# Performance work log

Hardware: AMD Instinct MI355X
Metric: run time of the kernel (lower is better)

Reference implementation:

```python
import jax, jax.numpy as jnp
import numpy as np

DIM_MODEL = 1024
DIM_K = 1024
DIM_V = 1024


def setup_inputs() -> dict:
    key = jax.random.key(0)
    ks = jax.random.split(key, 7)
    B, S = 4, 2048
    scale = 1.0 / np.sqrt(DIM_MODEL)
    return {
        "x": jax.random.normal(ks[0], (B, S, DIM_MODEL), dtype=jnp.float32),
        # weights stored [in, out] (transpose of torch Linear.weight)
        "Wq": jax.random.normal(ks[1], (DIM_MODEL, DIM_K), dtype=jnp.float32) * scale,
        "Wk": jax.random.normal(ks[2], (DIM_MODEL, DIM_K), dtype=jnp.float32) * scale,
        "Wv": jax.random.normal(ks[3], (DIM_MODEL, DIM_V), dtype=jnp.float32) * scale,
        "Wo": jax.random.normal(ks[4], (DIM_V, DIM_MODEL), dtype=jnp.float32) * (1.0 / np.sqrt(DIM_V)),
        "ln2_gamma": jnp.ones((DIM_MODEL,), dtype=jnp.float32),
        "ln2_beta": jnp.zeros((DIM_MODEL,), dtype=jnp.float32),
    }


def _layernorm(x, gamma, beta, eps=1e-5):
    mu = jnp.mean(x, axis=-1, keepdims=True)
    var = jnp.var(x, axis=-1, keepdims=True)
    return (x - mu) * jax.lax.rsqrt(var + eps) * gamma + beta


def reference(x, Wq, Wk, Wv, Wo, ln2_gamma, ln2_beta):
    # single-head attention, x: [B,S,D]
    q = jnp.einsum("bsd,dk->bsk", x, Wq)
    k = jnp.einsum("bsd,dk->bsk", x, Wk)
    v = jnp.einsum("bsd,dv->bsv", x, Wv)
    scores = jnp.einsum("bqk,bsk->bqs", q, k) / jnp.sqrt(jnp.asarray(DIM_K, x.dtype))
    attn = jax.nn.softmax(scores, axis=-1)  # [B,S,S]
    ctx = jnp.einsum("bqs,bsv->bqv", attn, v)
    hidden = jnp.einsum("bqv,vd->bqd", ctx, Wo)
    hidden = _layernorm(hidden, ln2_gamma, ln2_beta)
    return hidden
```

## Files before the change

### kernel.cpp

```cpp
#include <hip/hip_runtime.h>
#include <hip/hip_bf16.h>
#include <stdint.h>

typedef __bf16 bf16;
typedef __attribute__((ext_vector_type(8))) __bf16 bf16x8;
typedef __attribute__((ext_vector_type(4))) __bf16 bf16x4;
typedef __attribute__((ext_vector_type(4))) float f32x4;

#define AS1 __attribute__((address_space(1)))
#define AS3 __attribute__((address_space(3)))

__device__ __forceinline__ void gl_lds16(const void* g, void* l) {
  __builtin_amdgcn_global_load_lds((const AS1 uint32_t*)g, (AS3 uint32_t*)l, 16, 0, 0);
}

template <typename OUT, int MODE>
__global__ __launch_bounds__(256) void gemm_bt(
    const bf16* __restrict__ Abase, const bf16* __restrict__ Bbase,
    OUT* __restrict__ Cbase, int K, int lda, int ldb, int ldc,
    long long sA, long long sB, long long sC, float alpha,
    float* __restrict__ lsum) {
  __shared__ bf16 As[128 * 64];
  __shared__ bf16 Bs[128 * 64];
  const int z = blockIdx.z;
  const bf16* A = Abase + (long long)z * sA;
  const bf16* B = Bbase + (long long)z * sB;
  OUT* C = Cbase + (long long)z * sC;
  const int m0 = blockIdx.y * 128, n0 = blockIdx.x * 128;
  const int t = threadIdx.x;
  const int lane = t & 63, wave = t >> 6;
  const int wm = (wave >> 1) * 64, wn = (wave & 1) * 64;
  const int quad = lane >> 4, r = lane & 15;

  const int srow = t >> 3;
  const int schunk = (t & 7) ^ (srow & 7);
  const bf16* ga = A + (long long)(m0 + srow) * lda + schunk * 8;
  const bf16* gb = B + (long long)(n0 + srow) * ldb + schunk * 8;
  char* la = (char*)As + t * 16;
  char* lb = (char*)Bs + t * 16;

  f32x4 acc[4][4] = {};

  for (int k0 = 0; k0 < K; k0 += 64) {
    __syncthreads();
#pragma unroll
    for (int rd = 0; rd < 4; rd++) {
      gl_lds16(ga + (long long)(32 * rd) * lda, la + rd * 4096);
      gl_lds16(gb + (long long)(32 * rd) * ldb, lb + rd * 4096);
    }
    ga += 64;
    gb += 64;
    __syncthreads();

#pragma unroll
    for (int kk = 0; kk < 2; kk++) {
      bf16x8 af[4], bfr[4];
      const int csa = ((kk * 4 + quad) ^ (r & 7)) * 16;
      const char* pa = (const char*)As + (wm + r) * 128 + csa;
      const char* pb = (const char*)Bs + (wn + r) * 128 + csa;
#pragma unroll
      for (int i = 0; i < 4; i++) af[i] = *(const bf16x8*)(pa + i * 2048);
#pragma unroll
      for (int j = 0; j < 4; j++) bfr[j] = *(const bf16x8*)(pb + j * 2048);
#pragma unroll
      for (int i = 0; i < 4; i++)
#pragma unroll
        for (int j = 0; j < 4; j++)
          acc[i][j] = __builtin_amdgcn_mfma_f32_16x16x32_bf16(af[i], bfr[j],
                                                              acc[i][j], 0, 0, 0);
    }
  }

#pragma unroll
  for (int i = 0; i < 4; i++) {
    const int row0 = m0 + wm + i * 16 + quad * 4;
    float rsum[4] = {0.f, 0.f, 0.f, 0.f};
    float inv[4];
    if constexpr (MODE == 2) {
#pragma unroll
      for (int rg = 0; rg < 4; rg++)
        inv[rg] = 1.f / lsum[(long long)z * 2048 + row0 + rg];
    }
#pragma unroll
    for (int j = 0; j < 4; j++) {
      const int col = n0 + wn + j * 16 + r;
#pragma unroll
      for (int rg = 0; rg < 4; rg++) {
        float v = acc[i][j][rg] * alpha;
        if constexpr (MODE == 1) {
          bf16 eb = (bf16)__expf(v);
          C[(long long)(row0 + rg) * ldc + col] = (OUT)eb;
          rsum[rg] += (float)eb;
        } else if constexpr (MODE == 2) {
          C[(long long)(row0 + rg) * ldc + col] = (OUT)(v * inv[rg]);
        } else {
          C[(long long)(row0 + rg) * ldc + col] = (OUT)v;
        }
      }
    }
    if constexpr (MODE == 1) {
#pragma unroll
      for (int rg = 0; rg < 4; rg++) {
#pragma unroll
        for (int off = 8; off >= 1; off >>= 1)
          rsum[rg] += __shfl_xor(rsum[rg], off);
        if (r == 0)
          atomicAdd(&lsum[(long long)z * 2048 + row0 + rg], rsum[rg]);
      }
    }
  }
}

__global__ __launch_bounds__(256) void cvt_f32_bf16(
    const float* __restrict__ in, bf16* __restrict__ out, long long n8,
    float* __restrict__ lsum) {
  if (blockIdx.x < 32) lsum[blockIdx.x * 256 + threadIdx.x] = 0.f;
  long long i = (long long)blockIdx.x * 256 + threadIdx.x;
  if (i >= n8) return;
  const float4* p = (const float4*)in;
  float4 a = p[i * 2], b = p[i * 2 + 1];
  bf16x8 o;
  o[0] = (bf16)a.x; o[1] = (bf16)a.y; o[2] = (bf16)a.z; o[3] = (bf16)a.w;
  o[4] = (bf16)b.x; o[5] = (bf16)b.y; o[6] = (bf16)b.z; o[7] = (bf16)b.w;
  ((bf16x8*)out)[i] = o;
}

__global__ __launch_bounds__(256) void transpose_w4(
    const float* __restrict__ Wq, const float* __restrict__ Wk,
    const float* __restrict__ Wv, const float* __restrict__ Wo,
    bf16* __restrict__ Wcat, bf16* __restrict__ Wot) {
  __shared__ float tile[32][33];
  const int z = blockIdx.z;
  const float* W = (z == 0) ? Wq : (z == 1) ? Wk : (z == 2) ? Wv : Wo;
  bf16* dst = (z < 3) ? (Wcat + (long long)z * 1024 * 1024) : Wot;
  int bx = blockIdx.x * 32, by = blockIdx.y * 32;
  int tx = threadIdx.x & 31, ty = threadIdx.x >> 5;
#pragma unroll
  for (int i = 0; i < 32; i += 8)
    tile[ty + i][tx] = W[(long long)(by + ty + i) * 1024 + bx + tx];
  __syncthreads();
#pragma unroll
  for (int i = 0; i < 32; i += 8)
    dst[(long long)(bx + ty + i) * 1024 + by + tx] = (bf16)tile[tx][ty + i];
}

__global__ __launch_bounds__(256) void transpose_v(
    const bf16* __restrict__ V, bf16* __restrict__ Vt, int ldsrc,
    long long sV) {
  __shared__ bf16 tile[32][33];
  const bf16* Vb = V + (long long)blockIdx.z * sV;
  bf16* Vtb = Vt + (long long)blockIdx.z * 1024 * 2048;
  int bx = blockIdx.x * 32, by = blockIdx.y * 32;
  int tx = threadIdx.x & 31, ty = threadIdx.x >> 5;
#pragma unroll
  for (int i = 0; i < 32; i += 8)
    tile[ty + i][tx] = Vb[(long long)(by + ty + i) * ldsrc + bx + tx];
  __syncthreads();
#pragma unroll
  for (int i = 0; i < 32; i += 8)
    Vtb[(long long)(bx + ty + i) * 2048 + by + tx] = tile[tx][ty + i];
}

__global__ __launch_bounds__(256) void layernorm_rows(
    const bf16* __restrict__ H, const float* __restrict__ gamma,
    const float* __restrict__ beta, float* __restrict__ O) {
  const long long row = blockIdx.x;
  const bf16* h = H + row * 1024;
  float* o = O + row * 1024;
  const int t = threadIdx.x;
  const int lane = t & 63, wave = t >> 6;
  bf16x4 hv = ((const bf16x4*)h)[t];
  float v[4] = {(float)hv[0], (float)hv[1], (float)hv[2], (float)hv[3]};
  float s = v[0] + v[1] + v[2] + v[3];
  float ss = v[0] * v[0] + v[1] * v[1] + v[2] * v[2] + v[3] * v[3];
#pragma unroll
  for (int off = 32; off >= 1; off >>= 1) {
    s += __shfl_xor(s, off);
    ss += __shfl_xor(ss, off);
  }
  __shared__ float rs[4], rss[4];
  if (lane == 0) {
    rs[wave] = s;
    rss[wave] = ss;
  }
  __syncthreads();
  s = rs[0] + rs[1] + rs[2] + rs[3];
  ss = rss[0] + rss[1] + rss[2] + rss[3];
  const float mean = s * (1.f / 1024.f);
  const float var = ss * (1.f / 1024.f) - mean * mean;
  const float rstd = rsqrtf(var + 1e-5f);
  float4 g = ((const float4*)gamma)[t];
  float4 bb = ((const float4*)beta)[t];
  float4 rr;
  rr.x = (v[0] - mean) * rstd * g.x + bb.x;
  rr.y = (v[1] - mean) * rstd * g.y + bb.y;
  rr.z = (v[2] - mean) * rstd * g.z + bb.z;
  rr.w = (v[3] - mean) * rstd * g.w + bb.w;
  ((float4*)o)[t] = rr;
}

extern "C" void kernel_launch(void* const* d_in, const int* in_sizes, int n_in,
                              void* d_out, int out_size, void* d_ws,
                              size_t ws_size, hipStream_t stream) {
  const float* x = (const float*)d_in[0];
  const float* Wq = (const float*)d_in[1];
  const float* Wk = (const float*)d_in[2];
  const float* Wv = (const float*)d_in[3];
  const float* Wo = (const float*)d_in[4];
  const float* gamma = (const float*)d_in[5];
  const float* beta = (const float*)d_in[6];
  float* out = (float*)d_out;

  char* ws = (char*)d_ws;
  const size_t MB = 1024ull * 1024ull;
  bf16* Xb = (bf16*)(ws + 0);
  bf16* Wcat = (bf16*)(ws + 16 * MB);
  bf16* Wot = (bf16*)(ws + 22 * MB);
  bf16* QKV = (bf16*)(ws + 24 * MB);
  bf16* Vt = (bf16*)(ws + 72 * MB);
  bf16* expS = (bf16*)(ws + 88 * MB);
  float* lsum = (float*)(ws + 120 * MB);
  bf16* ctx = (bf16*)(ws + 121 * MB);
  bf16* Hd = (bf16*)(ws + 137 * MB);

  const long long bQKV = 2048LL * 3072;

  cvt_f32_bf16<<<4096, 256, 0, stream>>>(x, Xb, 8192LL * 1024 / 8, lsum);
  transpose_w4<<<dim3(32, 32, 4), 256, 0, stream>>>(Wq, Wk, Wv, Wo, Wcat, Wot);

  gemm_bt<bf16, 0><<<dim3(24, 64, 1), 256, 0, stream>>>(
      Xb, Wcat, QKV, 1024, 1024, 1024, 3072, 0, 0, 0, 1.f, nullptr);

  transpose_v<<<dim3(32, 64, 4), 256, 0, stream>>>(QKV + 2048, Vt, 3072, bQKV);

  gemm_bt<bf16, 1><<<dim3(16, 16, 4), 256, 0, stream>>>(
      QKV, QKV + 1024, expS, 1024, 3072, 3072, 2048, bQKV, bQKV,
      2048 * 2048LL, 0.03125f, lsum);

  gemm_bt<bf16, 2><<<dim3(8, 16, 4), 256, 0, stream>>>(
      expS, Vt, ctx, 2048, 2048, 2048, 1024, 2048 * 2048LL, 1024 * 2048LL,
      2048 * 1024LL, 1.f, lsum);

  gemm_bt<bf16, 0><<<dim3(8, 64, 1), 256, 0, stream>>>(
      ctx, Wot, Hd, 1024, 1024, 1024, 1024, 0, 0, 0, 1.f, nullptr);

  layernorm_rows<<<8192, 256, 0, stream>>>(Hd, gamma, beta, out);
}
```

Baseline: 311.9 us.

## Fuse V transpose into QKV GEMM, merge prep kernels, use 64-row tiles

The QKV GEMM epilogue now writes V-column blocks transposed into Vt through an LDS staging tile, which removes the separate transpose_v kernel and its extra read and write of V. The input conversion and the weight transposes are merged into one prep launch to save a kernel launch. The PV and output-projection GEMMs switch to a 64x128 tile kernel, doubling the grid size to improve CU occupancy on the small-grid GEMMs. In exchange the QKV GEMM does extra LDS work and an extra sync for the V blocks, and the smaller tiles reuse less data per block.

Measured after the change: 301.9 us. 3.2% less time.

```diff
diff --git a/kernel.cpp b/kernel.cpp
--- a/kernel.cpp
+++ b/kernel.cpp
@@ -14,18 +14,17 @@
   __builtin_amdgcn_global_load_lds((const AS1 uint32_t*)g, (AS3 uint32_t*)l, 16, 0, 0);
 }
 
-template <typename OUT, int MODE>
-__global__ __launch_bounds__(256) void gemm_bt(
+template <int MODE>
+__global__ __launch_bounds__(256) void gemm128(
     const bf16* __restrict__ Abase, const bf16* __restrict__ Bbase,
-    OUT* __restrict__ Cbase, int K, int lda, int ldb, int ldc,
+    bf16* __restrict__ Cbase, int K, int lda, int ldb, int ldc,
     long long sA, long long sB, long long sC, float alpha,
-    float* __restrict__ lsum) {
-  __shared__ bf16 As[128 * 64];
-  __shared__ bf16 Bs[128 * 64];
+    float* __restrict__ lsum, bf16* __restrict__ Vt) {
+  extern __shared__ char smem[];
   const int z = blockIdx.z;
   const bf16* A = Abase + (long long)z * sA;
   const bf16* B = Bbase + (long long)z * sB;
-  OUT* C = Cbase + (long long)z * sC;
+  bf16* C = Cbase + (long long)z * sC;
   const int m0 = blockIdx.y * 128, n0 = blockIdx.x * 128;
   const int t = threadIdx.x;
   const int lane = t & 63, wave = t >> 6;
@@ -36,8 +35,8 @@
   const int schunk = (t & 7) ^ (srow & 7);
   const bf16* ga = A + (long long)(m0 + srow) * lda + schunk * 8;
   const bf16* gb = B + (long long)(n0 + srow) * ldb + schunk * 8;
-  char* la = (char*)As + t * 16;
-  char* lb = (char*)Bs + t * 16;
+  char* la = smem + t * 16;
+  char* lb = smem + 16384 + t * 16;
 
   f32x4 acc[4][4] = {};
 
@@ -56,8 +55,8 @@
     for (int kk = 0; kk < 2; kk++) {
       bf16x8 af[4], bfr[4];
       const int csa = ((kk * 4 + quad) ^ (r & 7)) * 16;
-      const char* pa = (const char*)As + (wm + r) * 128 + csa;
-      const char* pb = (const char*)Bs + (wn + r) * 128 + csa;
+      const char* pa = smem + (wm + r) * 128 + csa;
+      const char* pb = smem + 16384 + (wn + r) * 128 + csa;
 #pragma unroll
       for (int i = 0; i < 4; i++) af[i] = *(const bf16x8*)(pa + i * 2048);
 #pragma unroll
@@ -68,6 +67,36 @@
         for (int j = 0; j < 4; j++)
           acc[i][j] = __builtin_amdgcn_mfma_f32_16x16x32_bf16(af[i], bfr[j],
                                                               acc[i][j], 0, 0, 0);
+    }
+  }
+
+  if constexpr (MODE == 3) {
+    if (blockIdx.x >= 16) {
+      bf16* T = (bf16*)smem;
+      __syncthreads();
+#pragma unroll
+      for (int i = 0; i < 4; i++)
+#pragma unroll
+        for (int j = 0; j < 4; j++)
+#pragma unroll
+          for (int rg = 0; rg < 4; rg++) {
+            const int m = wm + i * 16 + quad * 4 + rg;
+            const int n = wn + j * 16 + r;
+            T[n * 136 + m] = (bf16)acc[i][j][rg];
+          }
+      __syncthreads();
+      const int v0 = n0 - 2048;
+      const int zz = m0 >> 11;
+      const int s0l = m0 & 2047;
+      bf16* Vtb = Vt + (long long)zz * 1024 * 2048;
+      const int c = t & 15;
+#pragma unroll
+      for (int p = 0; p < 8; p++) {
+        const int n = p * 16 + (t >> 4);
+        bf16x8 val = *(const bf16x8*)(T + n * 136 + c * 8);
+        *(bf16x8*)(Vtb + (long long)(v0 + n) * 2048 + s0l + c * 8) = val;
+      }
+      return;
     }
   }
 
@@ -89,12 +118,12 @@
         float v = acc[i][j][rg] * alpha;
         if constexpr (MODE == 1) {
           bf16 eb = (bf16)__expf(v);
-          C[(long long)(row0 + rg) * ldc + col] = (OUT)eb;
+          C[(long long)(row0 + rg) * ldc + col] = eb;
           rsum[rg] += (float)eb;
         } else if constexpr (MODE == 2) {
-          C[(long long)(row0 + rg) * ldc + col] = (OUT)(v * inv[rg]);
+          C[(long long)(row0 + rg) * ldc + col] = (bf16)(v * inv[rg]);
         } else {
-          C[(long long)(row0 + rg) * ldc + col] = (OUT)v;
+          C[(long long)(row0 + rg) * ldc + col] = (bf16)v;
         }
       }
     }
@@ -111,54 +140,120 @@
   }
 }
 
-__global__ __launch_bounds__(256) void cvt_f32_bf16(
-    const float* __restrict__ in, bf16* __restrict__ out, long long n8,
+template <int MODE>
+__global__ __launch_bounds__(256) void gemm64(
+    const bf16* __restrict__ Abase, const bf16* __restrict__ Bbase,
+    bf16* __restrict__ Cbase, int K, int lda, int ldb, int ldc,
+    long long sA, long long sB, long long sC, float alpha,
     float* __restrict__ lsum) {
-  if (blockIdx.x < 32) lsum[blockIdx.x * 256 + threadIdx.x] = 0.f;
-  long long i = (long long)blockIdx.x * 256 + threadIdx.x;
-  if (i >= n8) return;
-  const float4* p = (const float4*)in;
-  float4 a = p[i * 2], b = p[i * 2 + 1];
-  bf16x8 o;
-  o[0] = (bf16)a.x; o[1] = (bf16)a.y; o[2] = (bf16)a.z; o[3] = (bf16)a.w;
-  o[4] = (bf16)b.x; o[5] = (bf16)b.y; o[6] = (bf16)b.z; o[7] = (bf16)b.w;
-  ((bf16x8*)out)[i] = o;
-}
-
-__global__ __launch_bounds__(256) void transpose_w4(
-    const float* __restrict__ Wq, const float* __restrict__ Wk,
-    const float* __restrict__ Wv, const float* __restrict__ Wo,
-    bf16* __restrict__ Wcat, bf16* __restrict__ Wot) {
+  extern __shared__ char smem[];
+  const int z = blockIdx.z;
+  const bf16* A = Abase + (long long)z * sA;
+  const bf16* B = Bbase + (long long)z * sB;
+  bf16* C = Cbase + (long long)z * sC;
+  const int m0 = blockIdx.y * 64, n0 = blockIdx.x * 128;
+  const int t = threadIdx.x;
+  const int lane = t & 63, wave = t >> 6;
+  const int wm = (wave >> 1) * 32, wn = (wave & 1) * 64;
+  const int quad = lane >> 4, r = lane & 15;
+
+  const int srow = t >> 3;
+  const int schunk = (t & 7) ^ (srow & 7);
+  const bf16* ga = A + (long long)(m0 + srow) * lda + schunk * 8;
+  const bf16* gb = B + (long long)(n0 + srow) * ldb + schunk * 8;
+  char* la = smem + t * 16;
+  char* lb = smem + 8192 + t * 16;
+
+  f32x4 acc[2][4] = {};
+
+  for (int k0 = 0; k0 < K; k0 += 64) {
+    __syncthreads();
+#pragma unroll
+    for (int rd = 0; rd < 2; rd++)
+      gl_lds16(ga + (long long)(32 * rd) * lda, la + rd * 4096);
+#pragma unroll
+    for (int rd = 0; rd < 4; rd++)
+      gl_lds16(gb + (long long)(32 * rd) * ldb, lb + rd * 4096);
+    ga += 64;
+    gb += 64;
+    __syncthreads();
+
+#pragma unroll
+    for (int kk = 0; kk < 2; kk++) {
+      bf16x8 af[2], bfr[4];
+      const int csa = ((kk * 4 + quad) ^ (r & 7)) * 16;
+      const char* pa = smem + (wm + r) * 128 + csa;
+      const char* pb = smem + 8192 + (wn + r) * 128 + csa;
+#pragma unroll
+      for (int i = 0; i < 2; i++) af[i] = *(const bf16x8*)(pa + i * 2048);
+#pragma unroll
+      for (int j = 0; j < 4; j++) bfr[j] = *(const bf16x8*)(pb + j * 2048);
+#pragma unroll
+      for (int i = 0; i < 2; i++)
+#pragma unroll
+        for (int j = 0; j < 4; j++)
+          acc[i][j] = __builtin_amdgcn_mfma_f32_16x16x32_bf16(af[i], bfr[j],
+                                                              acc[i][j], 0, 0, 0);
+    }
+  }
+
+#pragma unroll
+  for (int i = 0; i < 2; i++) {
+    const int row0 = m0 + wm + i * 16 + quad * 4;
+    float inv[4];
+    if constexpr (MODE == 2) {
+#pragma unroll
+      for (int rg = 0; rg < 4; rg++)
+        inv[rg] = 1.f / lsum[(long long)z * 2048 + row0 + rg];
+    }
+#pragma unroll
+    for (int j = 0; j < 4; j++) {
+      const int col = n0 + wn + j * 16 + r;
+#pragma unroll
+      for (int rg = 0; rg < 4; rg++) {
+        float v = acc[i][j][rg] * alpha;
+        if constexpr (MODE == 2) v *= inv[rg];
+        C[(long long)(row0 + rg) * ldc + col] = (bf16)v;
+      }
+    }
+  }
+}
+
+__global__ __launch_bounds__(256) void prep(
+    const float* __restrict__ x, const float* __restrict__ Wq,
+    const float* __restrict__ Wk, const float* __restrict__ Wv,
+    const float* __restrict__ Wo, bf16* __restrict__ Xb,
+    bf16* __restrict__ Wcat, bf16* __restrict__ Wot,
+    float* __restrict__ lsum) {
   __shared__ float tile[32][33];
-  const int z = blockIdx.z;
-  const float* W = (z == 0) ? Wq : (z == 1) ? Wk : (z == 2) ? Wv : Wo;
-  bf16* dst = (z < 3) ? (Wcat + (long long)z * 1024 * 1024) : Wot;
-  int bx = blockIdx.x * 32, by = blockIdx.y * 32;
-  int tx = threadIdx.x & 31, ty = threadIdx.x >> 5;
-#pragma unroll
-  for (int i = 0; i < 32; i += 8)
-    tile[ty + i][tx] = W[(long long)(by + ty + i) * 1024 + bx + tx];
-  __syncthreads();
-#pragma unroll
-  for (int i = 0; i < 32; i += 8)
-    dst[(long long)(bx + ty + i) * 1024 + by + tx] = (bf16)tile[tx][ty + i];
-}
-
-__global__ __launch_bounds__(256) void transpose_v(
-    const bf16* __restrict__ V, bf16* __restrict__ Vt, int ldsrc,
-    long long sV) {
-  __shared__ bf16 tile[32][33];
-  const bf16* Vb = V + (long long)blockIdx.z * sV;
-  bf16* Vtb = Vt + (long long)blockIdx.z * 1024 * 2048;
-  int bx = blockIdx.x * 32, by = blockIdx.y * 32;
-  int tx = threadIdx.x & 31, ty = threadIdx.x >> 5;
-#pragma unroll
-  for (int i = 0; i < 32; i += 8)
-    tile[ty + i][tx] = Vb[(long long)(by + ty + i) * ldsrc + bx + tx];
-  __syncthreads();
-#pragma unroll
-  for (int i = 0; i < 32; i += 8)
-    Vtb[(long long)(bx + ty + i) * 2048 + by + tx] = tile[tx][ty + i];
+  const int bx = blockIdx.x;
+  const int t = threadIdx.x;
+  if (bx < 4096) {
+    if (bx < 32) lsum[bx * 256 + t] = 0.f;
+    long long i = (long long)bx * 256 + t;
+    const float4* p = (const float4*)x;
+    float4 a = p[i * 2], b = p[i * 2 + 1];
+    bf16x8 o;
+    o[0] = (bf16)a.x; o[1] = (bf16)a.y; o[2] = (bf16)a.z; o[3] = (bf16)a.w;
+    o[4] = (bf16)b.x; o[5] = (bf16)b.y; o[6] = (bf16)b.z; o[7] = (bf16)b.w;
+    ((bf16x8*)Xb)[i] = o;
+  } else {
+    int idx = bx - 4096;
+    const int zw = idx >> 10;
+    idx &= 1023;
+    const int tiy = idx >> 5, tix = idx & 31;
+    const float* W = (zw == 0) ? Wq : (zw == 1) ? Wk : (zw == 2) ? Wv : Wo;
+    bf16* dst = (zw < 3) ? (Wcat + (long long)zw * 1024 * 1024) : Wot;
+    const int bx0 = tix * 32, by0 = tiy * 32;
+    const int ttx = t & 31, tty = t >> 5;
+#pragma unroll
+    for (int i = 0; i < 32; i += 8)
+      tile[tty + i][ttx] = W[(long long)(by0 + tty + i) * 1024 + bx0 + ttx];
+    __syncthreads();
+#pragma unroll
+    for (int i = 0; i < 32; i += 8)
+      dst[(long long)(bx0 + tty + i) * 1024 + by0 + ttx] = (bf16)tile[ttx][tty + i];
+  }
 }
 
 __global__ __launch_bounds__(256) void layernorm_rows(
@@ -225,23 +320,20 @@
 
   const long long bQKV = 2048LL * 3072;
 
-  cvt_f32_bf16<<<4096, 256, 0, stream>>>(x, Xb, 8192LL * 1024 / 8, lsum);
-  transpose_w4<<<dim3(32, 32, 4), 256, 0, stream>>>(Wq, Wk, Wv, Wo, Wcat, Wot);
-
-  gemm_bt<bf16, 0><<<dim3(24, 64, 1), 256, 0, stream>>>(
-      Xb, Wcat, QKV, 1024, 1024, 1024, 3072, 0, 0, 0, 1.f, nullptr);
-
-  transpose_v<<<dim3(32, 64, 4), 256, 0, stream>>>(QKV + 2048, Vt, 3072, bQKV);
-
-  gemm_bt<bf16, 1><<<dim3(16, 16, 4), 256, 0, stream>>>(
+  prep<<<8192, 256, 0, stream>>>(x, Wq, Wk, Wv, Wo, Xb, Wcat, Wot, lsum);
+
+  gemm128<3><<<dim3(24, 64, 1), 256, 34816, stream>>>(
+      Xb, Wcat, QKV, 1024, 1024, 1024, 3072, 0, 0, 0, 1.f, nullptr, Vt);
+
+  gemm128<1><<<dim3(16, 16, 4), 256, 32768, stream>>>(
       QKV, QKV + 1024, expS, 1024, 3072, 3072, 2048, bQKV, bQKV,
-      2048 * 2048LL, 0.03125f, lsum);
-
-  gemm_bt<bf16, 2><<<dim3(8, 16, 4), 256, 0, stream>>>(
+      2048 * 2048LL, 0.03125f, lsum, nullptr);
+
+  gemm64<2><<<dim3(8, 32, 4), 256, 24576, stream>>>(
       expS, Vt, ctx, 2048, 2048, 2048, 1024, 2048 * 2048LL, 1024 * 2048LL,
       2048 * 1024LL, 1.f, lsum);
 
-  gemm_bt<bf16, 0><<<dim3(8, 64, 1), 256, 0, stream>>>(
+  gemm64<0><<<dim3(8, 128, 1), 256, 24576, stream>>>(
       ctx, Wot, Hd, 1024, 1024, 1024, 1024, 0, 0, 0, 1.f, nullptr);
 
   layernorm_rows<<<8192, 256, 0, stream>>>(Hd, gamma, beta, out);
```
